# Kernel optimization log

Hardware: AMD Instinct MI355X
Metric: run time of the kernel (lower is better)

The kernel has to match this reference:

```python
import jax, jax.numpy as jnp
import numpy as np

EMBED_DIM = 1024
NUM_TOKENS = 32
TOKEN_DIM = 32  # ceil(1024/32)
CODEBOOK_SIZE = 256
BATCH = 32768
BETA = 0.25


def setup_inputs() -> dict:
    key = jax.random.key(0)
    ks = jax.random.split(key, 6)
    lim_e = 1.0 / np.sqrt(EMBED_DIM)
    lim_d = 1.0 / np.sqrt(NUM_TOKENS * TOKEN_DIM)
    lim_c = 1.0 / CODEBOOK_SIZE
    return {
        "skills": jax.random.normal(ks[0], (BATCH, EMBED_DIM), jnp.float32),
        "enc_w": jax.random.uniform(ks[1], (NUM_TOKENS * TOKEN_DIM, EMBED_DIM), jnp.float32, -lim_e, lim_e),
        "enc_b": jax.random.uniform(ks[2], (NUM_TOKENS * TOKEN_DIM,), jnp.float32, -lim_e, lim_e),
        "codebook": jax.random.uniform(ks[3], (CODEBOOK_SIZE, TOKEN_DIM), jnp.float32, -lim_c, lim_c),
        "dec_w": jax.random.uniform(ks[4], (EMBED_DIM, NUM_TOKENS * TOKEN_DIM), jnp.float32, -lim_d, lim_d),
        "dec_b": jax.random.uniform(ks[5], (EMBED_DIM,), jnp.float32, -lim_d, lim_d),
    }


def reference(skills, enc_w, enc_b, codebook, dec_w, dec_b):
    B = skills.shape[0]
    # encoder linear -> [B, num_tokens, token_dim]
    projected = (skills @ enc_w.T + enc_b).reshape(B, NUM_TOKENS, TOKEN_DIM)
    flat = projected.reshape(-1, TOKEN_DIM)  # [B*T, d]
    # squared-euclidean distances to codebook entries: [B*T, K]
    dists = (
        jnp.sum(flat * flat, axis=1, keepdims=True)
        - 2.0 * flat @ codebook.T
        + jnp.sum(codebook * codebook, axis=1)[None, :]
    )
    codes = jnp.argmin(dists, axis=1)  # [B*T]
    quantized = codebook[codes].reshape(B, NUM_TOKENS, TOKEN_DIM)
    # straight-through estimator
    st = projected + jax.lax.stop_gradient(quantized - projected)
    commitment = jnp.mean((projected - jax.lax.stop_gradient(quantized)) ** 2)
    codebook_loss = jnp.mean((quantized - jax.lax.stop_gradient(projected)) ** 2)
    vq_loss = codebook_loss + BETA * commitment
    reconstructed = st.reshape(B, NUM_TOKENS * TOKEN_DIM) @ dec_w.T + dec_b
    recon_loss = jnp.mean((reconstructed - skills) ** 2)
    loss = vq_loss + recon_loss
    return reconstructed, codes.reshape(B, NUM_TOKENS), loss
```

## Files before the change

### kernel.cpp

```cpp
#include <hip/hip_runtime.h>
#include <hip/hip_bf16.h>
#include <float.h>

#define OUT_CODES_OFF (33554432UL)
#define OUT_LOSS_OFF  (34603008UL)
#define TAU 1e-5f
#define INV_N (1.0f/33554432.0f)

typedef __attribute__((ext_vector_type(8))) short s16x8;
typedef __attribute__((ext_vector_type(4))) float f32x4;

__device__ __forceinline__ unsigned short bf16r(float x) {
    unsigned int u = __float_as_uint(x);
    unsigned int r = (u + 0x7FFFu + ((u >> 16) & 1u)) >> 16;
    return (unsigned short)r;
}
__device__ __forceinline__ float bf16f(unsigned short h) {
    return __uint_as_float(((unsigned int)h) << 16);
}
__device__ __forceinline__ void split8r(float4 v0, float4 v1, s16x8& h, s16x8& l) {
    float xs[8] = {v0.x, v0.y, v0.z, v0.w, v1.x, v1.y, v1.z, v1.w};
    #pragma unroll
    for (int e = 0; e < 8; ++e) {
        unsigned int u = __float_as_uint(xs[e]);
        unsigned short hh = (unsigned short)(u >> 16);
        h[e] = (short)hh;
        l[e] = (short)bf16r(xs[e] - bf16f(hh));
    }
}

__device__ __forceinline__ void gld16(const unsigned short* g, unsigned short* l) {
    __builtin_amdgcn_global_load_lds(
        (const __attribute__((address_space(1))) unsigned int*)g,
        (__attribute__((address_space(3))) unsigned int*)l, 16, 0, 0);
}

__global__ void k_prep_split(const float* __restrict__ in,
                             unsigned short* __restrict__ ot)
{
    const int b = blockIdx.x, tid = threadIdx.x;
    const int rblk = b >> 5, kt = b & 31, r = tid >> 2, q = tid & 3;
    const float* src = in + (size_t)(rblk * 128 + r) * 1024 + kt * 32 + q * 8;
    float4 v0 = *(const float4*)src, v1 = *(const float4*)(src + 4);
    s16x8 h, l;
    split8r(v0, v1, h, l);
    unsigned short* dst = ot + (size_t)b * 8192 + q * 1024 + r * 8;
    *(s16x8*)dst = h;
    *(s16x8*)(dst + 4096) = l;
}

__global__ void k_prep_r(const float* __restrict__ in,
                         unsigned short* __restrict__ o,
                         int n8)
{
    const int i = blockIdx.x * 256 + threadIdx.x;
    if (i >= n8) return;
    const float4* p = (const float4*)(in + (size_t)i * 8);
    float4 v0 = p[0], v1 = p[1];
    float xs[8] = {v0.x, v0.y, v0.z, v0.w, v1.x, v1.y, v1.z, v1.w};
    s16x8 h;
    #pragma unroll
    for (int e = 0; e < 8; ++e) h[e] = (short)bf16r(xs[e]);
    *(s16x8*)(o + (size_t)i * 8) = h;
}

__launch_bounds__(512, 1)
__global__ void k_enc_gl(const unsigned short* __restrict__ At,
                         const unsigned short* __restrict__ Bt,
                         const float* __restrict__ enc_b,
                         const float* __restrict__ cb_g,
                         float* __restrict__ out)
{
    __shared__ __align__(16) unsigned short us[49664];

    const int tid = threadIdx.x;
    const int wg = blockIdx.x;
    const int xcd = wg & 7, slot = wg >> 3;
    const int rb = xcd * 32 + (slot >> 1), chf = slot & 1;
    const int r0 = rb * 128;
    const int wid = tid >> 6, lane = tid & 63;
    const int wm = wid >> 1, wn = wid & 1;
    const int mbase = wm * 32;
    const int lhi = lane >> 4, llo = lane & 15;

    if (tid < 256) {
        const float4* cr = (const float4*)&cb_g[tid * 32];
        float s = 0.f;
        #pragma unroll
        for (int i = 0; i < 8; ++i) {
            float4 v = cr[i];
            float c[4] = {v.x, v.y, v.z, v.w};
            #pragma unroll
            for (int e = 0; e < 4; ++e) {
                const int d = i * 4 + e, kc = d >> 3, e8 = d & 7;
                unsigned int u = __float_as_uint(c[e]);
                unsigned short hh = (unsigned short)(u >> 16);
                us[32768 + kc * 2048 + tid * 8 + e8] = hh;
                us[40960 + kc * 2048 + tid * 8 + e8] = bf16r(c[e] - bf16f(hh));
                s = fmaf(c[e], c[e], s);
            }
        }
        *(float*)&us[49152 + tid * 2] = s;
    }
    {
        const unsigned short* gA = At + ((size_t)(rb * 32 + 0)) * 8192 + tid * 8;
        const unsigned short* gB = Bt + ((size_t)((chf * 4 + 0) * 32 + 0)) * 8192 + tid * 8;
        gld16(gA,        us + wid * 512);
        gld16(gA + 4096, us + 4096 + wid * 512);
        gld16(gB,        us + 8192 + wid * 512);
        gld16(gB + 4096, us + 12288 + wid * 512);
    }
    __syncthreads();

    float vq_local = 0.f;
    f32x4 acc[2][4];
    const int ntg_base = chf * 4;

    for (int it = 0; it < 128; ++it) {
        const int nt = it >> 5, kt = it & 31;
        if (kt == 0) {
            #pragma unroll
            for (int mf = 0; mf < 2; ++mf)
                #pragma unroll
                for (int nf = 0; nf < 4; ++nf) acc[mf][nf] = (f32x4)0.f;
        }
        if (it < 127) {
            const int tt = it + 1, ntn = tt >> 5, ktn = tt & 31;
            const int nb = (tt & 1) * 16384;
            const unsigned short* gA = At + ((size_t)(rb * 32 + ktn)) * 8192 + tid * 8;
            const unsigned short* gB = Bt + ((size_t)((ntg_base + ntn) * 32 + ktn)) * 8192 + tid * 8;
            gld16(gA,        us + nb + wid * 512);
            gld16(gA + 4096, us + nb + 4096 + wid * 512);
            gld16(gB,        us + nb + 8192 + wid * 512);
            gld16(gB + 4096, us + nb + 12288 + wid * 512);
        }
        {
            const int cb0 = (it & 1) * 16384;
            s16x8 ah[2], al[2];
            #pragma unroll
            for (int mf = 0; mf < 2; ++mf) {
                const int row = mbase + mf * 16 + llo;
                ah[mf] = *(s16x8*)&us[cb0 + lhi * 1024 + row * 8];
                al[mf] = *(s16x8*)&us[cb0 + 4096 + lhi * 1024 + row * 8];
            }
            #pragma unroll
            for (int nf = 0; nf < 4; ++nf) {
                const int rowb = wn * 64 + nf * 16 + llo;
                s16x8 bh = *(s16x8*)&us[cb0 + 8192 + lhi * 1024 + rowb * 8];
                s16x8 bl = *(s16x8*)&us[cb0 + 12288 + lhi * 1024 + rowb * 8];
                #pragma unroll
                for (int mf = 0; mf < 2; ++mf) {
                    acc[mf][nf] = __builtin_amdgcn_mfma_f32_16x16x32_bf16(ah[mf], bh, acc[mf][nf], 0, 0, 0);
                    acc[mf][nf] = __builtin_amdgcn_mfma_f32_16x16x32_bf16(ah[mf], bl, acc[mf][nf], 0, 0, 0);
                    acc[mf][nf] = __builtin_amdgcn_mfma_f32_16x16x32_bf16(al[mf], bh, acc[mf][nf], 0, 0, 0);
                }
            }
        }

        if (kt == 31) {
            for (int c = 0; c < 2; ++c) {
                __syncthreads();
                if (wn == c) {
                    #pragma unroll
                    for (int nf = 0; nf < 4; ++nf) {
                        const int colh = nf * 16 + llo;
                        const int tlc = colh >> 5, d = colh & 31;
                        const int kc = d >> 3, e8 = d & 7;
                        const float bias = enc_b[chf * 512 + nt * 128 + c * 64 + colh];
                        #pragma unroll
                        for (int mf = 0; mf < 2; ++mf)
                            #pragma unroll
                            for (int r = 0; r < 4; ++r) {
                                const int m_local = mbase + mf * 16 + lhi * 4 + r;
                                float val = acc[mf][nf][r] + bias;
                                unsigned int u = __float_as_uint(val);
                                unsigned short hh = (unsigned short)(u >> 16);
                                const int tok = m_local * 2 + tlc;
                                us[16384 + kc * 2048 + tok * 8 + e8] = hh;
                                us[24576 + kc * 2048 + tok * 8 + e8] = bf16r(val - bf16f(hh));
                            }
                    }
                }
                __syncthreads();
                s16x8 fh[2], fl[2];
                #pragma unroll
                for (int gi = 0; gi < 2; ++gi) {
                    const int tokrow = (wid * 2 + gi) * 16 + llo;
                    fh[gi] = *(s16x8*)&us[16384 + lhi * 2048 + tokrow * 8];
                    fl[gi] = *(s16x8*)&us[24576 + lhi * 2048 + tokrow * 8];
                }
                float s1[2][4], s2[2][4]; int bj[2][4];
                #pragma unroll
                for (int gi = 0; gi < 2; ++gi)
                    #pragma unroll
                    for (int r = 0; r < 4; ++r) { s1[gi][r] = FLT_MAX; s2[gi][r] = FLT_MAX; bj[gi][r] = 0; }
                for (int jb = 0; jb < 16; ++jb) {
                    const int j = jb * 16 + llo;
                    s16x8 ch = *(s16x8*)&us[32768 + lhi * 2048 + j * 8];
                    s16x8 cl = *(s16x8*)&us[40960 + lhi * 2048 + j * 8];
                    const float cnv = *(const float*)&us[49152 + j * 2];
                    #pragma unroll
                    for (int gi = 0; gi < 2; ++gi) {
                        f32x4 sc = (f32x4)0.f;
                        sc = __builtin_amdgcn_mfma_f32_16x16x32_bf16(fh[gi], ch, sc, 0, 0, 0);
                        sc = __builtin_amdgcn_mfma_f32_16x16x32_bf16(fh[gi], cl, sc, 0, 0, 0);
                        sc = __builtin_amdgcn_mfma_f32_16x16x32_bf16(fl[gi], ch, sc, 0, 0, 0);
                        #pragma unroll
                        for (int r = 0; r < 4; ++r) {
                            float s = fmaf(-2.f, sc[r], cnv);
                            if (s < s1[gi][r])      { s2[gi][r] = s1[gi][r]; s1[gi][r] = s; bj[gi][r] = j; }
                            else if (s < s2[gi][r]) { s2[gi][r] = s; }
                        }
                    }
                }
                #pragma unroll
                for (int gi = 0; gi < 2; ++gi) {
                    float Fp = 0.f;
                    #pragma unroll
                    for (int e = 0; e < 8; ++e) {
                        float fv = bf16f((unsigned short)fh[gi][e]) + bf16f((unsigned short)fl[gi][e]);
                        Fp = fmaf(fv, fv, Fp);
                    }
                    Fp += __shfl_xor(Fp, 16);
                    Fp += __shfl_xor(Fp, 32);
                    #pragma unroll
                    for (int r = 0; r < 4; ++r) {
                        float a1 = s1[gi][r], a2 = s2[gi][r]; int aj = bj[gi][r];
                        #pragma unroll
                        for (int off = 1; off <= 8; off <<= 1) {
                            float o1 = __shfl_xor(a1, off);
                            float o2 = __shfl_xor(a2, off);
                            int   oj = __shfl_xor(aj, off);
                            if (o1 < a1) { a2 = fminf(a1, o2); a1 = o1; aj = oj; }
                            else         { a2 = fminf(o1, a2); }
                        }
                        const float Ft = __shfl(Fp, lhi * 4 + r);
                        if (llo == 0) {
                            const int tok_local = (wid * 2 + gi) * 16 + lhi * 4 + r;
                            const int row = tok_local >> 1, tlc2 = tok_local & 1;
                            const int t = chf * 16 + nt * 4 + c * 2 + tlc2;
                            float cv = (a2 - a1 < TAU) ? (float)(aj + 512) : (float)aj;
                            out[OUT_CODES_OFF + (size_t)(r0 + row) * 32 + t] = cv;
                            vq_local += Ft + a1;
                        }
                    }
                }
            }
        }
        __syncthreads();
    }
    {
        float v = vq_local;
        #pragma unroll
        for (int off = 32; off >= 1; off >>= 1) v += __shfl_xor(v, off);
        if (lane == 0) atomicAdd(&out[OUT_LOSS_OFF], v * (1.25f * INV_N));
    }
}

__launch_bounds__(512, 1)
__global__ void k_enc_fb(const float* __restrict__ skills,
                         const float* __restrict__ enc_w,
                         const float* __restrict__ enc_b,
                         const float* __restrict__ cb_g,
                         float* __restrict__ out)
{
    __shared__ __align__(16) unsigned short us[40960];

    const int tid = threadIdx.x;
    const int rb = blockIdx.x >> 1, chf = blockIdx.x & 1;
    const int r0 = rb * 128;
    const int wid = tid >> 6, lane = tid & 63;
    const int wm = wid >> 1, wn = wid & 1;
    const int mbase = wm * 32;
    const int lhi = lane >> 4, llo = lane & 15;
    const int srow = tid >> 2, sq = tid & 3;

    if (tid < 256) {
        const float4* cr = (const float4*)&cb_g[tid * 32];
        float s = 0.f;
        #pragma unroll
        for (int i = 0; i < 8; ++i) {
            float4 v = cr[i];
            float c[4] = {v.x, v.y, v.z, v.w};
            #pragma unroll
            for (int e = 0; e < 4; ++e) {
                const int d = i * 4 + e;
                unsigned int u = __float_as_uint(c[e]);
                unsigned short hh = (unsigned short)(u >> 16);
                us[20480 + tid * 40 + d] = hh;
                us[30720 + tid * 40 + d] = bf16r(c[e] - bf16f(hh));
                s = fmaf(c[e], c[e], s);
            }
        }
        *(float*)&us[20480 + tid * 40 + 32] = s;
    }
    __syncthreads();

    float vq_local = 0.f;
    f32x4 acc[2][4];
    float4 ra0, ra1, rb0, rb1;
    {
        const float* ap = &skills[(size_t)(r0 + srow) * 1024 + sq * 8];
        ra0 = *(const float4*)ap; ra1 = *(const float4*)(ap + 4);
        const float* bp = &enc_w[(size_t)(chf * 512 + srow) * 1024 + sq * 8];
        rb0 = *(const float4*)bp; rb1 = *(const float4*)(bp + 4);
    }

    for (int it = 0; it < 128; ++it) {
        const int nt = it >> 5, kt = it & 31;
        if (kt == 0) {
            #pragma unroll
            for (int mf = 0; mf < 2; ++mf)
                #pragma unroll
                for (int nf = 0; nf < 4; ++nf) acc[mf][nf] = (f32x4)0.f;
        }
        __syncthreads();
        {
            s16x8 h, l;
            split8r(ra0, ra1, h, l);
            *(s16x8*)&us[srow * 40 + sq * 8] = h;
            *(s16x8*)&us[5120 + srow * 40 + sq * 8] = l;
            split8r(rb0, rb1, h, l);
            *(s16x8*)&us[10240 + srow * 40 + sq * 8] = h;
            *(s16x8*)&us[15360 + srow * 40 + sq * 8] = l;
        }
        __syncthreads();
        if (it < 127) {
            const int it2 = it + 1, nt2 = it2 >> 5, kt2 = it2 & 31;
            const float* ap = &skills[(size_t)(r0 + srow) * 1024 + kt2 * 32 + sq * 8];
            ra0 = *(const float4*)ap; ra1 = *(const float4*)(ap + 4);
            const float* bp = &enc_w[(size_t)(chf * 512 + nt2 * 128 + srow) * 1024 + kt2 * 32 + sq * 8];
            rb0 = *(const float4*)bp; rb1 = *(const float4*)(bp + 4);
        }
        {
            s16x8 ah[2], al[2];
            #pragma unroll
            for (int mf = 0; mf < 2; ++mf) {
                const int row = mbase + mf * 16 + llo;
                ah[mf] = *(s16x8*)&us[row * 40 + lhi * 8];
                al[mf] = *(s16x8*)&us[5120 + row * 40 + lhi * 8];
            }
            #pragma unroll
            for (int nf = 0; nf < 4; ++nf) {
                const int rowb = wn * 64 + nf * 16 + llo;
                s16x8 bh = *(s16x8*)&us[10240 + rowb * 40 + lhi * 8];
                s16x8 bl = *(s16x8*)&us[15360 + rowb * 40 + lhi * 8];
                #pragma unroll
                for (int mf = 0; mf < 2; ++mf) {
                    acc[mf][nf] = __builtin_amdgcn_mfma_f32_16x16x32_bf16(ah[mf], bh, acc[mf][nf], 0, 0, 0);
                    acc[mf][nf] = __builtin_amdgcn_mfma_f32_16x16x32_bf16(ah[mf], bl, acc[mf][nf], 0, 0, 0);
                    acc[mf][nf] = __builtin_amdgcn_mfma_f32_16x16x32_bf16(al[mf], bh, acc[mf][nf], 0, 0, 0);
                }
            }
        }

        if (kt == 31) {
            for (int c = 0; c < 2; ++c) {
                __syncthreads();
                if (wn == c) {
                    #pragma unroll
                    for (int nf = 0; nf < 4; ++nf) {
                        const int colh = nf * 16 + llo;
                        const int tlc = colh >> 5, d = colh & 31;
                        const float bias = enc_b[chf * 512 + nt * 128 + c * 64 + colh];
                        #pragma unroll
                        for (int mf = 0; mf < 2; ++mf)
                            #pragma unroll
                            for (int r = 0; r < 4; ++r) {
                                const int m_local = mbase + mf * 16 + lhi * 4 + r;
                                float val = acc[mf][nf][r] + bias;
                                unsigned int u = __float_as_uint(val);
                                unsigned short hh = (unsigned short)(u >> 16);
                                const int tok = m_local * 2 + tlc;
                                us[tok * 40 + d] = hh;
                                us[10240 + tok * 40 + d] = bf16r(val - bf16f(hh));
                            }
                    }
                }
                __syncthreads();
                s16x8 fh[2], fl[2];
                #pragma unroll
                for (int gi = 0; gi < 2; ++gi) {
                    const int tokrow = (wid * 2 + gi) * 16 + llo;
                    fh[gi] = *(s16x8*)&us[tokrow * 40 + lhi * 8];
                    fl[gi] = *(s16x8*)&us[10240 + tokrow * 40 + lhi * 8];
                }
                float s1[2][4], s2[2][4]; int bj[2][4];
                #pragma unroll
                for (int gi = 0; gi < 2; ++gi)
                    #pragma unroll
                    for (int r = 0; r < 4; ++r) { s1[gi][r] = FLT_MAX; s2[gi][r] = FLT_MAX; bj[gi][r] = 0; }
                for (int jb = 0; jb < 16; ++jb) {
                    const int j = jb * 16 + llo;
                    s16x8 ch = *(s16x8*)&us[20480 + j * 40 + lhi * 8];
                    s16x8 cl = *(s16x8*)&us[30720 + j * 40 + lhi * 8];
                    const float cnv = *(const float*)&us[20480 + j * 40 + 32];
                    #pragma unroll
                    for (int gi = 0; gi < 2; ++gi) {
                        f32x4 sc = (f32x4)0.f;
                        sc = __builtin_amdgcn_mfma_f32_16x16x32_bf16(fh[gi], ch, sc, 0, 0, 0);
                        sc = __builtin_amdgcn_mfma_f32_16x16x32_bf16(fh[gi], cl, sc, 0, 0, 0);
                        sc = __builtin_amdgcn_mfma_f32_16x16x32_bf16(fl[gi], ch, sc, 0, 0, 0);
                        #pragma unroll
                        for (int r = 0; r < 4; ++r) {
                            float s = fmaf(-2.f, sc[r], cnv);
                            if (s < s1[gi][r])      { s2[gi][r] = s1[gi][r]; s1[gi][r] = s; bj[gi][r] = j; }
                            else if (s < s2[gi][r]) { s2[gi][r] = s; }
                        }
                    }
                }
                #pragma unroll
                for (int gi = 0; gi < 2; ++gi) {
                    float Fp = 0.f;
                    #pragma unroll
                    for (int e = 0; e < 8; ++e) {
                        float fv = bf16f((unsigned short)fh[gi][e]) + bf16f((unsigned short)fl[gi][e]);
                        Fp = fmaf(fv, fv, Fp);
                    }
                    Fp += __shfl_xor(Fp, 16);
                    Fp += __shfl_xor(Fp, 32);
                    #pragma unroll
                    for (int r = 0; r < 4; ++r) {
                        float a1 = s1[gi][r], a2 = s2[gi][r]; int aj = bj[gi][r];
                        #pragma unroll
                        for (int off = 1; off <= 8; off <<= 1) {
                            float o1 = __shfl_xor(a1, off);
                            float o2 = __shfl_xor(a2, off);
                            int   oj = __shfl_xor(aj, off);
                            if (o1 < a1) { a2 = fminf(a1, o2); a1 = o1; aj = oj; }
                            else         { a2 = fminf(o1, a2); }
                        }
                        const float Ft = __shfl(Fp, lhi * 4 + r);
                        if (llo == 0) {
                            const int tok_local = (wid * 2 + gi) * 16 + lhi * 4 + r;
                            const int row = tok_local >> 1, tlc2 = tok_local & 1;
                            const int t = chf * 16 + nt * 4 + c * 2 + tlc2;
                            float cv = (a2 - a1 < TAU) ? (float)(aj + 512) : (float)aj;
                            out[OUT_CODES_OFF + (size_t)(r0 + row) * 32 + t] = cv;
                            vq_local += Ft + a1;
                        }
                    }
                }
            }
        }
    }
    {
        float v = vq_local;
        #pragma unroll
        for (int off = 32; off >= 1; off >>= 1) v += __shfl_xor(v, off);
        if (lane == 0) atomicAdd(&out[OUT_LOSS_OFF], v * (1.25f * INV_N));
    }
}

__launch_bounds__(256)
__global__ void k_fix(const float* __restrict__ skills,
                      const float* __restrict__ enc_w,
                      const float* __restrict__ enc_b,
                      const float* __restrict__ cb_g,
                      float* __restrict__ codes)
{
    __shared__ unsigned int cnt;
    __shared__ unsigned short list[256];

    const int tid = threadIdx.x;
    const int base = blockIdx.x * 256;

    if (tid == 0) cnt = 0;
    __syncthreads();
    {
        const int c = (int)codes[base + tid];
        if (c >= 512) {
            unsigned int ix = atomicAdd(&cnt, 1u);
            list[ix] = (unsigned short)tid;
        }
    }
    __syncthreads();
    const unsigned int n = cnt;
    if (n == 0) return;

    const int wv = tid >> 6, lane = tid & 63;
    const int d = lane & 31;

    for (unsigned int i = wv; i < n; i += 4) {
        const int tok = base + (int)list[i];
        const int row = tok >> 5;
        const int t   = tok & 31;

        const float4* s4 = (const float4*)&skills[(size_t)row * 1024];
        const float4* w4 = (const float4*)&enc_w[(size_t)(t * 32 + d) * 1024];
        float v1 = 0.f, v2 = 0.f, v3 = 0.f;
        for (int q = 0; q < 96; ++q) {
            float4 a = s4[q], b = w4[q];
            v1 = fmaf(a.x, b.x, v1); v1 = fmaf(a.y, b.y, v1);
            v1 = fmaf(a.z, b.z, v1); v1 = fmaf(a.w, b.w, v1);
        }
        for (int q = 96; q < 192; ++q) {
            float4 a = s4[q], b = w4[q];
            v2 = fmaf(a.x, b.x, v2); v2 = fmaf(a.y, b.y, v2);
            v2 = fmaf(a.z, b.z, v2); v2 = fmaf(a.w, b.w, v2);
        }
        for (int q = 192; q < 256; ++q) {
            float4 a = s4[q], b = w4[q];
            v3 = fmaf(a.x, b.x, v3); v3 = fmaf(a.y, b.y, v3);
            v3 = fmaf(a.z, b.z, v3); v3 = fmaf(a.w, b.w, v3);
        }
        const float pd = ((v1 + v2) + v3) + enc_b[t * 32 + d];

        float pv[32];
        #pragma unroll
        for (int dd = 0; dd < 32; ++dd) pv[dd] = __shfl(pd, dd);

        float F;
        {
            float s[32];
            #pragma unroll
            for (int dd = 0; dd < 32; ++dd) s[dd] = pv[dd] * pv[dd];
            float r[8];
            #pragma unroll
            for (int j = 0; j < 8; ++j) r[j] = ((s[j] + s[8+j]) + s[16+j]) + s[24+j];
            F = ((r[0] + r[1]) + (r[2] + r[3])) + ((r[4] + r[5]) + (r[6] + r[7]));
        }

        float bs = FLT_MAX; int bj = 0;
        for (int m = 0; m < 4; ++m) {
            const int j = m * 64 + lane;
            const float* cj = &cb_g[j * 32];
            float g = 0.f;
            #pragma unroll
            for (int dd = 0; dd < 32; ++dd) g = fmaf(pv[dd], cj[dd], g);
            float cs[32];
            #pragma unroll
            for (int dd = 0; dd < 32; ++dd) cs[dd] = cj[dd] * cj[dd];
            float r[8];
            #pragma unroll
            for (int jj = 0; jj < 8; ++jj) r[jj] = ((cs[jj] + cs[8+jj]) + cs[16+jj]) + cs[24+jj];
            float cn = ((r[0] + r[1]) + (r[2] + r[3])) + ((r[4] + r[5]) + (r[6] + r[7]));
            float dist = (F - 2.0f * g) + cn;
            if (dist < bs) { bs = dist; bj = j; }
        }
        #pragma unroll
        for (int off = 32; off >= 1; off >>= 1) {
            float os = __shfl_xor(bs, off);
            int   oj = __shfl_xor(bj, off);
            if (os < bs || (os == bs && oj < bj)) { bs = os; bj = oj; }
        }
        if (lane == 0) codes[tok] = (float)bj;
    }
}

template <bool PRED>
__launch_bounds__(512)
__global__ void k_dec(const float* __restrict__ skills,
                      const float* __restrict__ cb_g,
                      const unsigned short* __restrict__ cbb,
                      const float* __restrict__ dec_w,
                      const unsigned short* __restrict__ dwb,
                      const float* __restrict__ dec_b,
                      const float* __restrict__ codes,
                      float* __restrict__ recon,
                      float* __restrict__ loss_out)
{
    __shared__ unsigned short Qt[2][128][40], Wt[2][128][40];

    const int tid = threadIdx.x;
    const int r0 = (blockIdx.x >> 3) * 128;
    const int n0 = (blockIdx.x & 7) * 128;
    const int wid = tid >> 6, lane = tid & 63;
    const int wm = wid >> 1, wn = wid & 1;
    const int mbase = wm * 32, nbase = wn * 64;
    const int lhi = lane >> 4, llo = lane & 15;
    const int srow = tid >> 2, sq = tid & 3;

    f32x4 acc[2][4];
    #pragma unroll
    for (int mf = 0; mf < 2; ++mf)
        #pragma unroll
        for (int nf = 0; nf < 4; ++nf) acc[mf][nf] = (f32x4)0.f;

    s16x8 q16[2], w16[2];
    float4 q0[2], q1[2], w0[2], w1[2];

    #pragma unroll
    for (int ph = 0; ph < 2; ++ph) {
        const int cc = ((int)codes[(size_t)(r0 + srow) * 32 + ph]) & 255;
        if (PRED) {
            q16[ph] = *(const s16x8*)(cbb + cc * 32 + sq * 8);
            w16[ph] = *(const s16x8*)(dwb + (size_t)(n0 + srow) * 1024 + ph * 32 + sq * 8);
        } else {
            const float* cp = &cb_g[cc * 32 + sq * 8];
            q0[ph] = *(const float4*)cp; q1[ph] = *(const float4*)(cp + 4);
            const float* wp = &dec_w[(size_t)(n0 + srow) * 1024 + ph * 32 + sq * 8];
            w0[ph] = *(const float4*)wp; w1[ph] = *(const float4*)(wp + 4);
        }
    }

    for (int tt = 0; tt < 16; ++tt) {
        __syncthreads();
        #pragma unroll
        for (int ph = 0; ph < 2; ++ph) {
            if (PRED) {
                *(s16x8*)&Qt[ph][srow][sq * 8] = q16[ph];
                *(s16x8*)&Wt[ph][srow][sq * 8] = w16[ph];
            } else {
                float xs[8] = {q0[ph].x, q0[ph].y, q0[ph].z, q0[ph].w,
                               q1[ph].x, q1[ph].y, q1[ph].z, q1[ph].w};
                s16x8 h;
                #pragma unroll
                for (int e = 0; e < 8; ++e) h[e] = (short)bf16r(xs[e]);
                *(s16x8*)&Qt[ph][srow][sq * 8] = h;
                float ys[8] = {w0[ph].x, w0[ph].y, w0[ph].z, w0[ph].w,
                               w1[ph].x, w1[ph].y, w1[ph].z, w1[ph].w};
                #pragma unroll
                for (int e = 0; e < 8; ++e) h[e] = (short)bf16r(ys[e]);
                *(s16x8*)&Wt[ph][srow][sq * 8] = h;
            }
        }
        __syncthreads();
        if (tt < 15) {
            #pragma unroll
            for (int ph = 0; ph < 2; ++ph) {
                const int tn = tt * 2 + 2 + ph;
                const int cc = ((int)codes[(size_t)(r0 + srow) * 32 + tn]) & 255;
                if (PRED) {
                    q16[ph] = *(const s16x8*)(cbb + cc * 32 + sq * 8);
                    w16[ph] = *(const s16x8*)(dwb + (size_t)(n0 + srow) * 1024 + tn * 32 + sq * 8);
                } else {
                    const float* cp = &cb_g[cc * 32 + sq * 8];
                    q0[ph] = *(const float4*)cp; q1[ph] = *(const float4*)(cp + 4);
                    const float* wp = &dec_w[(size_t)(n0 + srow) * 1024 + tn * 32 + sq * 8];
                    w0[ph] = *(const float4*)wp; w1[ph] = *(const float4*)(wp + 4);
                }
            }
        }
        #pragma unroll
        for (int ph = 0; ph < 2; ++ph) {
            s16x8 aq[2], bw[4];
            #pragma unroll
            for (int mf = 0; mf < 2; ++mf)
                aq[mf] = *(s16x8*)&Qt[ph][mbase + mf * 16 + llo][lhi * 8];
            #pragma unroll
            for (int nf = 0; nf < 4; ++nf)
                bw[nf] = *(s16x8*)&Wt[ph][nbase + nf * 16 + llo][lhi * 8];
            #pragma unroll
            for (int mf = 0; mf < 2; ++mf)
                #pragma unroll
                for (int nf = 0; nf < 4; ++nf)
                    acc[mf][nf] = __builtin_amdgcn_mfma_f32_16x16x32_bf16(aq[mf], bw[nf], acc[mf][nf], 0, 0, 0);
        }
    }

    float lsum = 0.f;
    #pragma unroll
    for (int mf = 0; mf < 2; ++mf)
        #pragma unroll
        for (int nf = 0; nf < 4; ++nf) {
            const int col = n0 + nbase + nf * 16 + llo;
            const float bias = dec_b[col];
            #pragma unroll
            for (int r = 0; r < 4; ++r) {
                const int row = r0 + mbase + mf * 16 + lhi * 4 + r;
                float rv = acc[mf][nf][r] + bias;
                float dv = rv - skills[(size_t)row * 1024 + col];
                lsum = fmaf(dv, dv, lsum);
                recon[(size_t)row * 1024 + col] = rv;
            }
        }
    #pragma unroll
    for (int off = 32; off >= 1; off >>= 1) lsum += __shfl_xor(lsum, off);
    if (lane == 0) atomicAdd(loss_out, lsum * INV_N);
}

extern "C" void kernel_launch(void* const* d_in, const int* in_sizes, int n_in,
                              void* d_out, int out_size, void* d_ws, size_t ws_size,
                              hipStream_t stream)
{
    const float* skills = (const float*)d_in[0];
    const float* enc_w  = (const float*)d_in[1];
    const float* enc_b  = (const float*)d_in[2];
    const float* cbg    = (const float*)d_in[3];
    const float* dec_w  = (const float*)d_in[4];
    const float* dec_b  = (const float*)d_in[5];
    float* out = (float*)d_out;

    hipMemsetAsync(out + OUT_LOSS_OFF, 0, 4, stream);

    const size_t NEED_BIG = 4UL*1024*1024 + 2097152UL + 16384UL + 256UL;
    unsigned short* wsu16 = (unsigned short*)d_ws;

    if (ws_size >= NEED_BIG) {
        unsigned short* Btl = wsu16;
        unsigned short* dwb = wsu16 + 2097152UL;
        unsigned short* cbb = wsu16 + 3145728UL;
        unsigned short* Atl = (unsigned short*)out;

        k_prep_split<<<dim3(8192), dim3(512), 0, stream>>>(skills, Atl);
        k_prep_split<<<dim3(256),  dim3(512), 0, stream>>>(enc_w, Btl);
        k_enc_gl<<<dim3(512), dim3(512), 0, stream>>>(Atl, Btl, enc_b, cbg, out);
        k_fix<<<dim3(4096), dim3(256), 0, stream>>>(skills, enc_w, enc_b, cbg, out + OUT_CODES_OFF);
        k_prep_r<<<dim3(512), dim3(256), 0, stream>>>(dec_w, dwb, 131072);
        k_prep_r<<<dim3(4), dim3(256), 0, stream>>>(cbg, cbb, 1024);
        k_dec<true><<<dim3(2048), dim3(512), 0, stream>>>(skills, cbg, cbb, dec_w, dwb, dec_b,
                                                          out + OUT_CODES_OFF, out, out + OUT_LOSS_OFF);
    } else {
        k_enc_fb<<<dim3(512), dim3(512), 0, stream>>>(skills, enc_w, enc_b, cbg, out);
        k_fix<<<dim3(4096), dim3(256), 0, stream>>>(skills, enc_w, enc_b, cbg, out + OUT_CODES_OFF);
        const bool pred = (ws_size >= (2097152UL + 16384UL + 64UL));
        unsigned short* dwb = wsu16;
        unsigned short* cbb = wsu16 + 1048576UL;
        if (pred) {
            k_prep_r<<<dim3(512), dim3(256), 0, stream>>>(dec_w, dwb, 131072);
            k_prep_r<<<dim3(4), dim3(256), 0, stream>>>(cbg, cbb, 1024);
            k_dec<true><<<dim3(2048), dim3(512), 0, stream>>>(skills, cbg, cbb, dec_w, dwb, dec_b,
                                                              out + OUT_CODES_OFF, out, out + OUT_LOSS_OFF);
        } else {
            k_dec<false><<<dim3(2048), dim3(512), 0, stream>>>(skills, cbg, cbb, dec_w, dwb, dec_b,
                                                               out + OUT_CODES_OFF, out, out + OUT_LOSS_OFF);
        }
    }
}
```

Before: 809.3 us.

## Fuse skills bf16 hi/lo split into encoder GEMM A-tile loading

Removes the separate k_prep_split pass over the skills matrix. The encoder GEMM now loads fp32 skills rows straight into registers one stage ahead, splits them into bf16 hi/lo in-kernel and writes them to LDS. This saves a full write plus re-read of the split A matrix (about 128MB of traffic). The cost is extra VALU work and register-staged rather than direct-to-LDS loads. Each A tile is also now converted once per N pass (four times), which adds redundant conversion work.

```diff
diff --git a/kernel.cpp b/kernel.cpp
--- a/kernel.cpp
+++ b/kernel.cpp
@@ -65,7 +65,7 @@
 }
 
 __launch_bounds__(512, 1)
-__global__ void k_enc_gl(const unsigned short* __restrict__ At,
+__global__ void k_enc_gl(const float* __restrict__ skills,
                          const unsigned short* __restrict__ Bt,
                          const float* __restrict__ enc_b,
                          const float* __restrict__ cb_g,
@@ -82,6 +82,7 @@
     const int wm = wid >> 1, wn = wid & 1;
     const int mbase = wm * 32;
     const int lhi = lane >> 4, llo = lane & 15;
+    const int srow = tid >> 2, sq = tid & 3;
 
     if (tid < 256) {
         const float4* cr = (const float4*)&cb_g[tid * 32];
@@ -102,13 +103,20 @@
         }
         *(float*)&us[49152 + tid * 2] = s;
     }
+
+    float4 ra0, ra1;
     {
-        const unsigned short* gA = At + ((size_t)(rb * 32 + 0)) * 8192 + tid * 8;
+        const float* ap = &skills[(size_t)(r0 + srow) * 1024 + sq * 8];
+        ra0 = *(const float4*)ap; ra1 = *(const float4*)(ap + 4);
+        s16x8 h, l;
+        split8r(ra0, ra1, h, l);
+        *(s16x8*)&us[sq * 1024 + srow * 8] = h;
+        *(s16x8*)&us[4096 + sq * 1024 + srow * 8] = l;
         const unsigned short* gB = Bt + ((size_t)((chf * 4 + 0) * 32 + 0)) * 8192 + tid * 8;
-        gld16(gA,        us + wid * 512);
-        gld16(gA + 4096, us + 4096 + wid * 512);
         gld16(gB,        us + 8192 + wid * 512);
         gld16(gB + 4096, us + 12288 + wid * 512);
+        const float* ap1 = &skills[(size_t)(r0 + srow) * 1024 + 32 + sq * 8];
+        ra0 = *(const float4*)ap1; ra1 = *(const float4*)(ap1 + 4);
     }
     __syncthreads();
 
@@ -127,12 +135,20 @@
         if (it < 127) {
             const int tt = it + 1, ntn = tt >> 5, ktn = tt & 31;
             const int nb = (tt & 1) * 16384;
-            const unsigned short* gA = At + ((size_t)(rb * 32 + ktn)) * 8192 + tid * 8;
+            {
+                s16x8 h, l;
+                split8r(ra0, ra1, h, l);
+                *(s16x8*)&us[nb + sq * 1024 + srow * 8] = h;
+                *(s16x8*)&us[nb + 4096 + sq * 1024 + srow * 8] = l;
+            }
             const unsigned short* gB = Bt + ((size_t)((ntg_base + ntn) * 32 + ktn)) * 8192 + tid * 8;
-            gld16(gA,        us + nb + wid * 512);
-            gld16(gA + 4096, us + nb + 4096 + wid * 512);
             gld16(gB,        us + nb + 8192 + wid * 512);
             gld16(gB + 4096, us + nb + 12288 + wid * 512);
+            if (it < 126) {
+                const int t2 = it + 2, kt2 = t2 & 31;
+                const float* ap = &skills[(size_t)(r0 + srow) * 1024 + kt2 * 32 + sq * 8];
+                ra0 = *(const float4*)ap; ra1 = *(const float4*)(ap + 4);
+            }
         }
         {
             const int cb0 = (it & 1) * 16384;
@@ -691,11 +707,9 @@
         unsigned short* Btl = wsu16;
         unsigned short* dwb = wsu16 + 2097152UL;
         unsigned short* cbb = wsu16 + 3145728UL;
-        unsigned short* Atl = (unsigned short*)out;
-
-        k_prep_split<<<dim3(8192), dim3(512), 0, stream>>>(skills, Atl);
+
         k_prep_split<<<dim3(256),  dim3(512), 0, stream>>>(enc_w, Btl);
-        k_enc_gl<<<dim3(512), dim3(512), 0, stream>>>(Atl, Btl, enc_b, cbg, out);
+        k_enc_gl<<<dim3(512), dim3(512), 0, stream>>>(skills, Btl, enc_b, cbg, out);
         k_fix<<<dim3(4096), dim3(256), 0, stream>>>(skills, enc_w, enc_b, cbg, out + OUT_CODES_OFF);
         k_prep_r<<<dim3(512), dim3(256), 0, stream>>>(dec_w, dwb, 131072);
         k_prep_r<<<dim3(4), dim3(256), 0, stream>>>(cbg, cbb, 1024);
```

Result: no change. 814.4 us (+0.6%).
